# Kernel tuning notes

Measured on AMD Instinct MI355X. Metric: run time of the kernel, lower is better.

Reference implementation:

```python
import jax, jax.numpy as jnp
import numpy as np

N_NODES = 100000
N_EDGES = 1600000
F_IN = 128
EMB = 128
HEADS = 4
D_HEAD = EMB // HEADS
HIDDEN = 256
BATCH = 2048
CANDS = 16  # distractors + 1


def setup_inputs() -> dict:
    key = jax.random.key(0)
    ks = jax.random.split(key, 10)
    message = jax.random.normal(ks[0], (BATCH, HIDDEN), jnp.float32)
    x = jax.random.normal(ks[1], (N_NODES, F_IN), jnp.float32)
    edge_index = jax.random.randint(ks[2], (2, N_EDGES), 0, N_NODES, jnp.int64)
    indices = jax.random.randint(ks[3], (BATCH * CANDS,), 0, N_NODES, jnp.int64)
    s = 1.0 / np.sqrt(F_IN)
    W = jax.random.normal(ks[4], (F_IN, HEADS, D_HEAD), jnp.float32) * s
    att_src = jax.random.normal(ks[5], (HEADS, D_HEAD), jnp.float32) * s
    att_dst = jax.random.normal(ks[6], (HEADS, D_HEAD), jnp.float32) * s
    bias = jnp.zeros((EMB,), jnp.float32)
    fc_w = jax.random.normal(ks[7], (EMB, HIDDEN), jnp.float32) / np.sqrt(HIDDEN)
    fc_b = jnp.zeros((EMB,), jnp.float32)
    return {"message": message, "x": x, "edge_index": edge_index, "indices": indices,
            "W": W, "att_src": att_src, "att_dst": att_dst, "bias": bias,
            "fc_w": fc_w, "fc_b": fc_b}


def _gat(x, edge_index, W, att_src, att_dst, bias):
    N = x.shape[0]
    loops = jnp.arange(N, dtype=edge_index.dtype)
    src = jnp.concatenate([edge_index[0], loops])  # self-loops (PyG default)
    dst = jnp.concatenate([edge_index[1], loops])
    Wx = jnp.einsum('nf,fhd->nhd', x, W)                      # [N,H,D]
    a_s = (Wx * att_src).sum(-1)                              # [N,H]
    a_d = (Wx * att_dst).sum(-1)
    e = jax.nn.leaky_relu(a_s[src] + a_d[dst], 0.2)           # [E,H]
    m = jax.ops.segment_max(e, dst, num_segments=N)           # segment softmax
    ex = jnp.exp(e - m[dst])
    den = jax.ops.segment_sum(ex, dst, num_segments=N)
    alpha = ex / den[dst]
    out = jax.ops.segment_sum(alpha[:, :, None] * Wx[src], dst, num_segments=N)
    return out.reshape(N, -1) + bias                          # [N, H*D]


def reference(message, x, edge_index, indices, W, att_src, att_dst, bias, fc_w, fc_b):
    h = _gat(x, edge_index, W, att_src, att_dst, bias)        # [N, EMB]
    B = message.shape[0]
    emb = h[indices].reshape(B, -1, h.shape[-1])              # [B,C,EMB]
    msg = message @ fc_w.T + fc_b                             # [B,EMB]
    dots = jnp.einsum('bce,be->bc', emb, msg)                 # bmm scoring
    amax = jnp.abs(dots).max()
    tie = ((jnp.abs(dots) - amax) < 1e-10).astype(dots.dtype)
    noise = jax.random.normal(jax.random.key(42), dots.shape, dots.dtype)
    dots = dots + tie * amax * 1e-5 * noise
    return jax.nn.log_softmax(dots, axis=1)
```

## Files before the change

kernel.cpp:

```cpp
#include <hip/hip_runtime.h>
#include <stdint.h>
#include <stddef.h>

#define N_NODES 100000
#define N_EDGES 1600000
#define F_IN 128
#define EMB 128
#define HEADS 4
#define D_HEAD 32
#define HIDDEN 256
#define BATCH 2048
#define CANDS 16
#define NSLOTS 32768
#define WXBLOCKS 782
#define WTROWS 144
#define STR 136

typedef __attribute__((ext_vector_type(8))) short v8s;
typedef __attribute__((ext_vector_type(4))) float v4f;

__device__ __forceinline__ unsigned short f2bs(float f) {
  unsigned int u = __builtin_bit_cast(unsigned int, f);
  u = (u + 0x7fffu + ((u >> 16) & 1u)) >> 16;
  return (unsigned short)u;
}
__device__ __forceinline__ float bs2f(unsigned int s) {
  unsigned int u = (s & 0xffffu) << 16;
  return __builtin_bit_cast(float, u);
}

__global__ __launch_bounds__(256) void k_prep(const float* __restrict__ W,
                                              const float* __restrict__ att_src,
                                              const float* __restrict__ att_dst,
                                              unsigned short* __restrict__ Wtp,
                                              const int* __restrict__ idx,
                                              int* __restrict__ nidx,
                                              int* __restrict__ cnt) {
  int i = blockIdx.x * 256 + threadIdx.x;
  if (i < 128 * STR) {
    int r = i / STR, c = i - r * STR;
    Wtp[i] = (c < 128) ? f2bs(W[c * 128 + r]) : (unsigned short)0;
  } else if (i < WTROWS * STR) {
    int ii = i - 128 * STR;
    int r = ii / STR, c = ii - r * STR;
    unsigned short v = 0;
    if (c < 128 && r < 8) {
      const float* att = (r < 4) ? att_src : att_dst;
      int hh = r & 3;
      float s = 0.f;
#pragma unroll
      for (int d = 0; d < 32; ++d) s += W[c * 128 + hh * 32 + d] * att[hh * 32 + d];
      v = f2bs(s);
    }
    Wtp[i] = v;
  }
  if (i < NSLOTS) {
    cnt[i] = 0;
    nidx[idx[i]] = i;
  }
}

__global__ __launch_bounds__(256) void k_scatmsg(const int* __restrict__ ei,
                                                 const int* __restrict__ idx,
                                                 const int* __restrict__ nidx,
                                                 int* __restrict__ cnt,
                                                 int* __restrict__ srclist,
                                                 const float* __restrict__ message,
                                                 const float* __restrict__ fc_w,
                                                 const float* __restrict__ fc_b,
                                                 float* __restrict__ msg) {
  __shared__ float Sm[8][256];
  __shared__ float red[8 * 128];
  int tid = threadIdx.x;
  if (blockIdx.x < 256) {
    int b0 = blockIdx.x * 8;
    for (int i = tid; i < 8 * 256; i += 256)
      Sm[i >> 8][i & 255] = message[(size_t)b0 * 256 + i];
    __syncthreads();
    int e = tid & 127, half = tid >> 7;
    float acc[8];
#pragma unroll
    for (int r = 0; r < 8; ++r) acc[r] = 0.f;
    const float* wrow = fc_w + (size_t)e * 256 + half * 128;
    for (int k = 0; k < 128; k += 4) {
      float4 w4 = *(const float4*)(wrow + k);
#pragma unroll
      for (int r = 0; r < 8; ++r) {
        float4 m4 = *(const float4*)(&Sm[r][half * 128 + k]);
        acc[r] += m4.x * w4.x + m4.y * w4.y + m4.z * w4.z + m4.w * w4.w;
      }
    }
    __syncthreads();
    if (half == 0) {
#pragma unroll
      for (int r = 0; r < 8; ++r) red[r * 128 + e] = acc[r];
    }
    __syncthreads();
    if (half == 1) {
#pragma unroll
      for (int r = 0; r < 8; ++r) red[r * 128 + e] += acc[r];
    }
    __syncthreads();
    for (int i = tid; i < 1024; i += 256)
      msg[(size_t)b0 * 128 + i] = red[i] + fc_b[i & 127];
  } else {
    int e = (blockIdx.x - 256) * 256 + tid;
    if (e >= N_EDGES) return;
    int dst = ei[N_EDGES + e];
    unsigned int ni = (unsigned int)nidx[dst];
    if (ni >= NSLOTS) return;
    if (idx[ni] != dst) return;
    int pos = atomicAdd(&cnt[ni], 1);
    if (pos < 64) srclist[ni * 64 + pos] = ei[e];
  }
}

__global__ __launch_bounds__(256) void k_wx(const float* __restrict__ x,
                                            const unsigned short* __restrict__ Wtp,
                                            unsigned short* __restrict__ Wx,
                                            float* __restrict__ a_s,
                                            float* __restrict__ a_d) {
  __shared__ unsigned short wt[WTROWS * STR];
  int tid = threadIdx.x;

  {
    const uint4* s = (const uint4*)Wtp;
    uint4* d = (uint4*)wt;
#pragma unroll
    for (int it = 0; it < 10; ++it) {
      int i = it * 256 + tid;
      if (i < WTROWS * STR / 8) d[i] = s[i];
    }
  }
  __syncthreads();

  int w = tid >> 6, lane = tid & 63;
  int m = lane & 15, quad = lane >> 4;

  for (int chunk = 0; chunk < 2; ++chunk) {
    int rbase = blockIdx.x * 128 + chunk * 64;
    int gr = rbase + w * 16 + m;
    if (gr >= N_NODES) gr = N_NODES - 1;
    const float* xrow = x + (size_t)gr * 128;

    v8s afrag[4];
#pragma unroll
    for (int t = 0; t < 4; ++t) {
      const float4* gp = (const float4*)(xrow + t * 32 + quad * 8);
      float4 f0 = gp[0], f1 = gp[1];
      v8s a;
      a[0] = (short)f2bs(f0.x); a[1] = (short)f2bs(f0.y);
      a[2] = (short)f2bs(f0.z); a[3] = (short)f2bs(f0.w);
      a[4] = (short)f2bs(f1.x); a[5] = (short)f2bs(f1.y);
      a[6] = (short)f2bs(f1.z); a[7] = (short)f2bs(f1.w);
      afrag[t] = a;
    }

    v4f acc[9];
#pragma unroll
    for (int nt = 0; nt < 9; ++nt) {
      v4f a0 = {0.f, 0.f, 0.f, 0.f};
      const unsigned short* brow = wt + (size_t)(nt * 16 + m) * STR;
#pragma unroll
      for (int t = 0; t < 4; ++t) {
        v8s b = *(const v8s*)(brow + t * 32 + quad * 8);
        a0 = __builtin_amdgcn_mfma_f32_16x16x32_bf16(afrag[t], b, a0, 0, 0, 0);
      }
      acc[nt] = a0;
    }

#pragma unroll
    for (int r = 0; r < 4; ++r) {
      int orow = rbase + w * 16 + quad * 4 + r;
      if (orow < N_NODES) {
        if (m < 4) a_s[(size_t)orow * 4 + m] = acc[8][r];
        else if (m < 8) a_d[(size_t)orow * 4 + m - 4] = acc[8][r];
        v8s v;
#pragma unroll
        for (int nt = 0; nt < 8; ++nt) v[nt] = (short)f2bs(acc[nt][r]);
        *(v8s*)(&Wx[(size_t)orow * 128 + m * 8]) = v;
      }
    }
  }
}

__global__ __launch_bounds__(256) void k_aggscore(const float* __restrict__ a_s,
                                                  const float* __restrict__ a_d,
                                                  const unsigned short* __restrict__ Wx,
                                                  const int* __restrict__ idx,
                                                  const int* __restrict__ nidx,
                                                  const int* __restrict__ cnt,
                                                  const int* __restrict__ srclist,
                                                  const int* __restrict__ ei,
                                                  const float* __restrict__ bias,
                                                  const float* __restrict__ msg,
                                                  float* __restrict__ out) {
  __shared__ int sS[16][64];
  __shared__ float sW[16][64 * 4];
  __shared__ float sdots[16];
  int w = threadIdx.x >> 6, lane = threadIdx.x & 63;
  int q = lane >> 4, li = lane & 15;
  int wq = w * 4 + q;
  int b = blockIdx.x;
  int wid = b * 16 + wq;
  int dst = idx[wid];
  int ci = nidx[dst];
  int degRaw = cnt[ci];
  int deg = degRaw < 64 ? degRaw : 64;
  float4 ad4 = *(const float4*)(a_d + (size_t)dst * 4);
  float4 dsum = {0.f, 0.f, 0.f, 0.f};
  for (int t = li; t < deg; t += 16) {
    int sv = srclist[ci * 64 + t];
    float4 as = *(const float4*)(a_s + (size_t)sv * 4);
    float e0 = as.x + ad4.x; e0 = e0 > 0.f ? e0 : 0.2f * e0;
    float e1 = as.y + ad4.y; e1 = e1 > 0.f ? e1 : 0.2f * e1;
    float e2 = as.z + ad4.z; e2 = e2 > 0.f ? e2 : 0.2f * e2;
    float e3 = as.w + ad4.w; e3 = e3 > 0.f ? e3 : 0.2f * e3;
    float4 w4;
    w4.x = __expf(e0); w4.y = __expf(e1);
    w4.z = __expf(e2); w4.w = __expf(e3);
    sS[wq][t] = sv;
    *(float4*)(&sW[wq][t * 4]) = w4;
    dsum.x += w4.x; dsum.y += w4.y; dsum.z += w4.z; dsum.w += w4.w;
  }
  asm volatile("s_waitcnt lgkmcnt(0)" ::: "memory");

#pragma unroll
  for (int o = 8; o >= 1; o >>= 1) {
    dsum.x += __shfl_xor(dsum.x, o);
    dsum.y += __shfl_xor(dsum.y, o);
    dsum.z += __shfl_xor(dsum.z, o);
    dsum.w += __shfl_xor(dsum.w, o);
  }

  float4 as4 = *(const float4*)(a_s + (size_t)dst * 4);
  float s0 = as4.x + ad4.x; s0 = s0 > 0.f ? s0 : 0.2f * s0;
  float s1 = as4.y + ad4.y; s1 = s1 > 0.f ? s1 : 0.2f * s1;
  float s2 = as4.z + ad4.z; s2 = s2 > 0.f ? s2 : 0.2f * s2;
  float s3 = as4.w + ad4.w; s3 = s3 > 0.f ? s3 : 0.2f * s3;
  float wself[4];
  wself[0] = __expf(s0); wself[1] = __expf(s1);
  wself[2] = __expf(s2); wself[3] = __expf(s3);
  float den4[4];
  den4[0] = dsum.x + wself[0]; den4[1] = dsum.y + wself[1];
  den4[2] = dsum.z + wself[2]; den4[3] = dsum.w + wself[3];

  float acc[8];
  {
    uint4 u = *(const uint4*)(Wx + (size_t)dst * 128 + li * 8);
    acc[0] = wself[0] * bs2f(u.x); acc[1] = wself[0] * bs2f(u.x >> 16);
    acc[2] = wself[1] * bs2f(u.y); acc[3] = wself[1] * bs2f(u.y >> 16);
    acc[4] = wself[2] * bs2f(u.z); acc[5] = wself[2] * bs2f(u.z >> 16);
    acc[6] = wself[3] * bs2f(u.w); acc[7] = wself[3] * bs2f(u.w >> 16);
  }

  if (degRaw > 64) {
    den4[0] = wself[0]; den4[1] = wself[1];
    den4[2] = wself[2]; den4[3] = wself[3];
    for (int e = 0; e < N_EDGES; ++e) {
      if (ei[N_EDGES + e] == dst) {
        int sv = ei[e];
        float4 as = *(const float4*)(a_s + (size_t)sv * 4);
        float e0 = as.x + ad4.x; e0 = e0 > 0.f ? e0 : 0.2f * e0;
        float e1 = as.y + ad4.y; e1 = e1 > 0.f ? e1 : 0.2f * e1;
        float e2 = as.z + ad4.z; e2 = e2 > 0.f ? e2 : 0.2f * e2;
        float e3 = as.w + ad4.w; e3 = e3 > 0.f ? e3 : 0.2f * e3;
        float wa0 = __expf(e0), wa1 = __expf(e1);
        float wa2 = __expf(e2), wa3 = __expf(e3);
        den4[0] += wa0; den4[1] += wa1; den4[2] += wa2; den4[3] += wa3;
        uint4 u = *(const uint4*)(Wx + (size_t)sv * 128 + li * 8);
        acc[0] += wa0 * bs2f(u.x); acc[1] += wa0 * bs2f(u.x >> 16);
        acc[2] += wa1 * bs2f(u.y); acc[3] += wa1 * bs2f(u.y >> 16);
        acc[4] += wa2 * bs2f(u.z); acc[5] += wa2 * bs2f(u.z >> 16);
        acc[6] += wa3 * bs2f(u.w); acc[7] += wa3 * bs2f(u.w >> 16);
      }
    }
  } else {
#pragma unroll 4
    for (int j = 0; j < deg; ++j) {
      int s = sS[wq][j];
      float4 wv = *(const float4*)(&sW[wq][j * 4]);
      uint4 u = *(const uint4*)(Wx + (size_t)s * 128 + li * 8);
      acc[0] += wv.x * bs2f(u.x); acc[1] += wv.x * bs2f(u.x >> 16);
      acc[2] += wv.y * bs2f(u.y); acc[3] += wv.y * bs2f(u.y >> 16);
      acc[4] += wv.z * bs2f(u.z); acc[5] += wv.z * bs2f(u.z >> 16);
      acc[6] += wv.w * bs2f(u.w); acc[7] += wv.w * bs2f(u.w >> 16);
    }
  }

  float invh[4];
  invh[0] = 1.0f / den4[0]; invh[1] = 1.0f / den4[1];
  invh[2] = 1.0f / den4[2]; invh[3] = 1.0f / den4[3];
  const float* mrow = msg + (size_t)b * 128;
  float dp = 0.f;
#pragma unroll
  for (int k = 0; k < 8; ++k) {
    int c = k * 16 + li;
    dp += (acc[k] * invh[k >> 1] + bias[c]) * mrow[c];
  }
#pragma unroll
  for (int o = 8; o >= 1; o >>= 1) dp += __shfl_xor(dp, o);
  if (li == 0) sdots[wq] = dp;
  __syncthreads();
  if (threadIdx.x < 16) {
    float d = sdots[threadIdx.x];
    float mx = d;
#pragma unroll
    for (int o = 1; o < 16; o <<= 1) mx = fmaxf(mx, __shfl_xor(mx, o));
    float ex = __expf(d - mx);
    float sum = ex;
#pragma unroll
    for (int o = 1; o < 16; o <<= 1) sum += __shfl_xor(sum, o);
    out[b * 16 + threadIdx.x] = d - mx - __logf(sum);
  }
}

extern "C" void kernel_launch(void* const* d_in, const int* in_sizes, int n_in,
                              void* d_out, int out_size, void* d_ws, size_t ws_size,
                              hipStream_t stream) {
  (void)in_sizes; (void)n_in; (void)out_size; (void)ws_size;
  const float* message = (const float*)d_in[0];
  const float* x       = (const float*)d_in[1];
  const int*   ei      = (const int*)d_in[2];
  const int*   indices = (const int*)d_in[3];
  const float* W       = (const float*)d_in[4];
  const float* att_src = (const float*)d_in[5];
  const float* att_dst = (const float*)d_in[6];
  const float* bias    = (const float*)d_in[7];
  const float* fc_w    = (const float*)d_in[8];
  const float* fc_b    = (const float*)d_in[9];
  float* out = (float*)d_out;

  char* p = (char*)d_ws;
  auto alloc = [&](size_t bytes) -> char* {
    char* r = p;
    p += (bytes + 255) & ~(size_t)255;
    return r;
  };
  unsigned short* Wx = (unsigned short*)alloc((size_t)N_NODES * 128 * 2);
  float* a_s = (float*)alloc((size_t)N_NODES * 4 * 4);
  float* a_d = (float*)alloc((size_t)N_NODES * 4 * 4);
  unsigned short* Wtp = (unsigned short*)alloc((size_t)WTROWS * STR * 2);
  int* nidx      = (int*)alloc((size_t)N_NODES * 4);
  int* cnt       = (int*)alloc((size_t)NSLOTS * 4);
  int* srclist   = (int*)alloc((size_t)NSLOTS * 64 * 4);
  float* msg     = (float*)alloc((size_t)BATCH * 128 * 4);

  k_prep<<<128, 256, 0, stream>>>(W, att_src, att_dst, Wtp, indices, nidx, cnt);
  k_scatmsg<<<256 + N_EDGES / 256, 256, 0, stream>>>(ei, indices, nidx, cnt, srclist,
                                                     message, fc_w, fc_b, msg);
  k_wx<<<WXBLOCKS, 256, 0, stream>>>(x, Wtp, Wx, a_s, a_d);
  k_aggscore<<<BATCH, 256, 0, stream>>>(a_s, a_d, Wx, indices, nidx, cnt, srclist,
                                        ei, bias, msg, out);
}
```

Baseline: 186.7 us.

## Merge Wx projection, message FC and edge scatter into one launch

Fuses the k_wx and k_scatmsg kernels into a single k_mega launch whose block ranges dispatch to the Wx MFMA projection, the message linear layer, or the edge scatter. Shared memory is unioned across the roles. The edge scatter now handles four edges per thread with an int4 load of destinations. The aim is to remove a launch and let independent work overlap on the GPU, at the cost of every block reserving the larger shared-memory footprint, which may lower occupancy for the scatter blocks.

```diff
diff --git a/kernel.cpp b/kernel.cpp
--- a/kernel.cpp
+++ b/kernel.cpp
@@ -12,9 +12,14 @@
 #define BATCH 2048
 #define CANDS 16
 #define NSLOTS 32768
-#define WXBLOCKS 782
 #define WTROWS 144
 #define STR 136
+
+#define WX_BLOCKS 782
+#define MSG_BLOCKS 256
+#define EDGE_QUADS 400000
+#define EDGE_BLOCKS 1563
+#define MEGA_BLOCKS (WX_BLOCKS + MSG_BLOCKS + EDGE_BLOCKS)
 
 typedef __attribute__((ext_vector_type(8))) short v8s;
 typedef __attribute__((ext_vector_type(4))) float v4f;
@@ -60,22 +65,91 @@
   }
 }
 
-__global__ __launch_bounds__(256) void k_scatmsg(const int* __restrict__ ei,
-                                                 const int* __restrict__ idx,
-                                                 const int* __restrict__ nidx,
-                                                 int* __restrict__ cnt,
-                                                 int* __restrict__ srclist,
-                                                 const float* __restrict__ message,
-                                                 const float* __restrict__ fc_w,
-                                                 const float* __restrict__ fc_b,
-                                                 float* __restrict__ msg) {
-  __shared__ float Sm[8][256];
-  __shared__ float red[8 * 128];
+__global__ __launch_bounds__(256) void k_mega(const float* __restrict__ x,
+                                              const unsigned short* __restrict__ Wtp,
+                                              unsigned short* __restrict__ Wx,
+                                              float* __restrict__ a_s,
+                                              float* __restrict__ a_d,
+                                              const int* __restrict__ ei,
+                                              const int* __restrict__ idx,
+                                              const int* __restrict__ nidx,
+                                              int* __restrict__ cnt,
+                                              int* __restrict__ srclist,
+                                              const float* __restrict__ message,
+                                              const float* __restrict__ fc_w,
+                                              const float* __restrict__ fc_b,
+                                              float* __restrict__ msg) {
+  __shared__ unsigned short smem[WTROWS * STR];
   int tid = threadIdx.x;
-  if (blockIdx.x < 256) {
-    int b0 = blockIdx.x * 8;
+  int bx = blockIdx.x;
+
+  if (bx < WX_BLOCKS) {
+    unsigned short* wt = smem;
+    {
+      const uint4* s = (const uint4*)Wtp;
+      uint4* d = (uint4*)wt;
+#pragma unroll
+      for (int it = 0; it < 10; ++it) {
+        int i = it * 256 + tid;
+        if (i < WTROWS * STR / 8) d[i] = s[i];
+      }
+    }
+    __syncthreads();
+
+    int w = tid >> 6, lane = tid & 63;
+    int m = lane & 15, quad = lane >> 4;
+
+    for (int chunk = 0; chunk < 2; ++chunk) {
+      int rbase = bx * 128 + chunk * 64;
+      int gr = rbase + w * 16 + m;
+      if (gr >= N_NODES) gr = N_NODES - 1;
+      const float* xrow = x + (size_t)gr * 128;
+
+      v8s afrag[4];
+#pragma unroll
+      for (int t = 0; t < 4; ++t) {
+        const float4* gp = (const float4*)(xrow + t * 32 + quad * 8);
+        float4 f0 = gp[0], f1 = gp[1];
+        v8s a;
+        a[0] = (short)f2bs(f0.x); a[1] = (short)f2bs(f0.y);
+        a[2] = (short)f2bs(f0.z); a[3] = (short)f2bs(f0.w);
+        a[4] = (short)f2bs(f1.x); a[5] = (short)f2bs(f1.y);
+        a[6] = (short)f2bs(f1.z); a[7] = (short)f2bs(f1.w);
+        afrag[t] = a;
+      }
+
+      v4f acc[9];
+#pragma unroll
+      for (int nt = 0; nt < 9; ++nt) {
+        v4f a0 = {0.f, 0.f, 0.f, 0.f};
+        const unsigned short* brow = wt + (size_t)(nt * 16 + m) * STR;
+#pragma unroll
+        for (int t = 0; t < 4; ++t) {
+          v8s b = *(const v8s*)(brow + t * 32 + quad * 8);
+          a0 = __builtin_amdgcn_mfma_f32_16x16x32_bf16(afrag[t], b, a0, 0, 0, 0);
+        }
+        acc[nt] = a0;
+      }
+
+#pragma unroll
+      for (int r = 0; r < 4; ++r) {
+        int orow = rbase + w * 16 + quad * 4 + r;
+        if (orow < N_NODES) {
+          if (m < 4) a_s[(size_t)orow * 4 + m] = acc[8][r];
+          else if (m < 8) a_d[(size_t)orow * 4 + m - 4] = acc[8][r];
+          v8s v;
+#pragma unroll
+          for (int nt = 0; nt < 8; ++nt) v[nt] = (short)f2bs(acc[nt][r]);
+          *(v8s*)(&Wx[(size_t)orow * 128 + m * 8]) = v;
+        }
+      }
+    }
+  } else if (bx < WX_BLOCKS + MSG_BLOCKS) {
+    float* Sm = (float*)smem;
+    float* red = ((float*)smem) + 2048;
+    int b0 = (bx - WX_BLOCKS) * 8;
     for (int i = tid; i < 8 * 256; i += 256)
-      Sm[i >> 8][i & 255] = message[(size_t)b0 * 256 + i];
+      Sm[i] = message[(size_t)b0 * 256 + i];
     __syncthreads();
     int e = tid & 127, half = tid >> 7;
     float acc[8];
@@ -86,7 +160,7 @@
       float4 w4 = *(const float4*)(wrow + k);
 #pragma unroll
       for (int r = 0; r < 8; ++r) {
-        float4 m4 = *(const float4*)(&Sm[r][half * 128 + k]);
+        float4 m4 = *(const float4*)(&Sm[r * 256 + half * 128 + k]);
         acc[r] += m4.x * w4.x + m4.y * w4.y + m4.z * w4.z + m4.w * w4.w;
       }
     }
@@ -104,81 +178,17 @@
     for (int i = tid; i < 1024; i += 256)
       msg[(size_t)b0 * 128 + i] = red[i] + fc_b[i & 127];
   } else {
-    int e = (blockIdx.x - 256) * 256 + tid;
-    if (e >= N_EDGES) return;
-    int dst = ei[N_EDGES + e];
-    unsigned int ni = (unsigned int)nidx[dst];
-    if (ni >= NSLOTS) return;
-    if (idx[ni] != dst) return;
-    int pos = atomicAdd(&cnt[ni], 1);
-    if (pos < 64) srclist[ni * 64 + pos] = ei[e];
-  }
-}
-
-__global__ __launch_bounds__(256) void k_wx(const float* __restrict__ x,
-                                            const unsigned short* __restrict__ Wtp,
-                                            unsigned short* __restrict__ Wx,
-                                            float* __restrict__ a_s,
-                                            float* __restrict__ a_d) {
-  __shared__ unsigned short wt[WTROWS * STR];
-  int tid = threadIdx.x;
-
-  {
-    const uint4* s = (const uint4*)Wtp;
-    uint4* d = (uint4*)wt;
-#pragma unroll
-    for (int it = 0; it < 10; ++it) {
-      int i = it * 256 + tid;
-      if (i < WTROWS * STR / 8) d[i] = s[i];
-    }
-  }
-  __syncthreads();
-
-  int w = tid >> 6, lane = tid & 63;
-  int m = lane & 15, quad = lane >> 4;
-
-  for (int chunk = 0; chunk < 2; ++chunk) {
-    int rbase = blockIdx.x * 128 + chunk * 64;
-    int gr = rbase + w * 16 + m;
-    if (gr >= N_NODES) gr = N_NODES - 1;
-    const float* xrow = x + (size_t)gr * 128;
-
-    v8s afrag[4];
-#pragma unroll
-    for (int t = 0; t < 4; ++t) {
-      const float4* gp = (const float4*)(xrow + t * 32 + quad * 8);
-      float4 f0 = gp[0], f1 = gp[1];
-      v8s a;
-      a[0] = (short)f2bs(f0.x); a[1] = (short)f2bs(f0.y);
-      a[2] = (short)f2bs(f0.z); a[3] = (short)f2bs(f0.w);
-      a[4] = (short)f2bs(f1.x); a[5] = (short)f2bs(f1.y);
-      a[6] = (short)f2bs(f1.z); a[7] = (short)f2bs(f1.w);
-      afrag[t] = a;
-    }
-
-    v4f acc[9];
-#pragma unroll
-    for (int nt = 0; nt < 9; ++nt) {
-      v4f a0 = {0.f, 0.f, 0.f, 0.f};
-      const unsigned short* brow = wt + (size_t)(nt * 16 + m) * STR;
-#pragma unroll
-      for (int t = 0; t < 4; ++t) {
-        v8s b = *(const v8s*)(brow + t * 32 + quad * 8);
-        a0 = __builtin_amdgcn_mfma_f32_16x16x32_bf16(afrag[t], b, a0, 0, 0, 0);
-      }
-      acc[nt] = a0;
-    }
-
-#pragma unroll
-    for (int r = 0; r < 4; ++r) {
-      int orow = rbase + w * 16 + quad * 4 + r;
-      if (orow < N_NODES) {
-        if (m < 4) a_s[(size_t)orow * 4 + m] = acc[8][r];
-        else if (m < 8) a_d[(size_t)orow * 4 + m - 4] = acc[8][r];
-        v8s v;
-#pragma unroll
-        for (int nt = 0; nt < 8; ++nt) v[nt] = (short)f2bs(acc[nt][r]);
-        *(v8s*)(&Wx[(size_t)orow * 128 + m * 8]) = v;
+    int e4 = (bx - WX_BLOCKS - MSG_BLOCKS) * 256 + tid;
+    if (e4 >= EDGE_QUADS) return;
+    int4 d4 = *(const int4*)(ei + N_EDGES + (size_t)e4 * 4);
+    int ds[4] = {d4.x, d4.y, d4.z, d4.w};
+#pragma unroll
+    for (int j = 0; j < 4; ++j) {
+      int dst = ds[j];
+      unsigned int ni = (unsigned int)nidx[dst];
+      if (ni < NSLOTS && idx[ni] == dst) {
+        int pos = atomicAdd(&cnt[ni], 1);
+        if (pos < 64) srclist[ni * 64 + pos] = ei[(size_t)e4 * 4 + j];
       }
     }
   }
@@ -347,9 +357,8 @@
   float* msg     = (float*)alloc((size_t)BATCH * 128 * 4);
 
   k_prep<<<128, 256, 0, stream>>>(W, att_src, att_dst, Wtp, indices, nidx, cnt);
-  k_scatmsg<<<256 + N_EDGES / 256, 256, 0, stream>>>(ei, indices, nidx, cnt, srclist,
-                                                     message, fc_w, fc_b, msg);
-  k_wx<<<WXBLOCKS, 256, 0, stream>>>(x, Wtp, Wx, a_s, a_d);
+  k_mega<<<MEGA_BLOCKS, 256, 0, stream>>>(x, Wtp, Wx, a_s, a_d, ei, indices, nidx,
+                                          cnt, srclist, message, fc_w, fc_b, msg);
   k_aggscore<<<BATCH, 256, 0, stream>>>(a_s, a_d, Wx, indices, nidx, cnt, srclist,
                                         ei, bias, msg, out);
 }
```

Result: faster. 180.8 us (-3.2%).
